# Kernel tuning notes

Measured on AMD Instinct MI355X. Metric: run time of the kernel, lower is better.

## Reference

```python
import jax, jax.numpy as jnp
import numpy as np

B, T, D, H = 2, 2048, 1024, 16
HS = D // H  # head_size = 64
EPS = 1e-5


def layer_norm(x, g, b):
    mu = jnp.mean(x, axis=-1, keepdims=True)
    var = jnp.var(x, axis=-1, keepdims=True)
    return (x - mu) * jax.lax.rsqrt(var + EPS) * g + b


def setup_inputs() -> dict:
    key = jax.random.key(0)
    ks = jax.random.split(key, 12)
    s_attn = 1.0 / np.sqrt(D)
    s_ff1 = 1.0 / np.sqrt(D)
    s_ff2 = 1.0 / np.sqrt(4 * D)
    return {
        "x": jax.random.normal(ks[0], (B, T, D), jnp.float32),
        "Wq": jax.random.normal(ks[1], (H, D, HS), jnp.float32) * s_attn,
        "Wk": jax.random.normal(ks[2], (H, D, HS), jnp.float32) * s_attn,
        "Wv": jax.random.normal(ks[3], (H, D, HS), jnp.float32) * s_attn,
        "Wo": jax.random.normal(ks[4], (H * HS, D), jnp.float32) * (1.0 / np.sqrt(H * HS)),
        "bo": jnp.zeros((D,), jnp.float32),
        "W1": jax.random.normal(ks[5], (D, 4 * D), jnp.float32) * s_ff1,
        "b1": jnp.zeros((4 * D,), jnp.float32),
        "W2": jax.random.normal(ks[6], (4 * D, D), jnp.float32) * s_ff2,
        "b2": jnp.zeros((D,), jnp.float32),
        "ln1_g": jnp.ones((D,), jnp.float32),
        "ln1_b": jnp.zeros((D,), jnp.float32),
        "ln2_g": jnp.ones((D,), jnp.float32),
        "ln2_b": jnp.zeros((D,), jnp.float32),
    }


def reference(x, Wq, Wk, Wv, Wo, bo, W1, b1, W2, b2, ln1_g, ln1_b, ln2_g, ln2_b):
    # --- self-attention on ln1(x) ---
    h = layer_norm(x, ln1_g, ln1_b)
    Q = jnp.einsum('bsd,hdk->bhsk', h, Wq)
    K = jnp.einsum('bsd,hdk->bhsk', h, Wk)
    V = jnp.einsum('bsd,hdk->bhsk', h, Wv)
    scores = jnp.einsum('bhqk,bhsk->bhqs', Q, K) * (HS ** -0.5)
    attn = jax.nn.softmax(scores, axis=-1)  # [B,H,T,T] non-causal, as in source
    out = jnp.einsum('bhqs,bhsk->bhqk', attn, V)
    out = out.transpose(0, 2, 1, 3).reshape(B, T, H * HS)  # concat heads
    sa = out @ Wo + bo
    x = x + sa
    # --- feed-forward on ln2(x) ---
    h2 = layer_norm(x, ln2_g, ln2_b)
    ff = jax.nn.relu(h2 @ W1 + b1) @ W2 + b2
    return x + ff
```

## Files before the change

kernel.cpp:

```cpp
#include <hip/hip_runtime.h>
#include <cstdint>
#include <cmath>

typedef __bf16 bf16;
typedef __bf16 bf16x8 __attribute__((ext_vector_type(8)));
typedef __bf16 bf16x4 __attribute__((ext_vector_type(4)));
typedef float  f32x4  __attribute__((ext_vector_type(4)));

#define B_   2
#define T_   2048
#define D_   1024
#define H_   16
#define HS_  64
#define NTOK (B_ * T_)

typedef __attribute__((address_space(1))) uint8_t* gp1_t;
typedef __attribute__((address_space(3))) uint8_t* lp3_t;
__device__ __forceinline__ void gl_lds16(const void* g, void* l) {
    __builtin_amdgcn_global_load_lds((gp1_t)(uintptr_t)g,
                                     (lp3_t)(uint32_t)(uintptr_t)l,
                                     16, 0, 0);
}

__device__ __forceinline__ f32x4 mfma16(bf16x8 a, bf16x8 b, f32x4 c) {
    return __builtin_amdgcn_mfma_f32_16x16x32_bf16(a, b, c, 0, 0, 0);
}

__global__ void tcast(const float* __restrict__ in, bf16* __restrict__ out,
                      int R, int C) {
    __shared__ float t[32][33];
    const int c0 = blockIdx.x * 32, r0 = blockIdx.y * 32;
    for (int i = 0; i < 4; i++) {
        int r = threadIdx.y + i * 8;
        t[r][threadIdx.x] = in[(size_t)(r0 + r) * C + c0 + threadIdx.x];
    }
    __syncthreads();
    for (int i = 0; i < 4; i++) {
        int rr = threadIdx.y + i * 8;
        out[(size_t)(c0 + rr) * R + r0 + threadIdx.x] = (bf16)t[threadIdx.x][rr];
    }
}

__global__ void qkv_pack(const float* __restrict__ Wq, const float* __restrict__ Wk,
                         const float* __restrict__ Wv, bf16* __restrict__ out) {
    const int z = blockIdx.z;
    const int qkv = z >> 4;
    const float* in = (qkv == 0 ? Wq : qkv == 1 ? Wk : Wv) + (size_t)(z & 15) * D_ * HS_;
    bf16* o = out + (size_t)z * HS_ * D_;
    __shared__ float t[32][33];
    const int c0 = blockIdx.x * 32, r0 = blockIdx.y * 32;
    for (int i = 0; i < 4; i++) {
        int r = threadIdx.y + i * 8;
        t[r][threadIdx.x] = in[(size_t)(r0 + r) * HS_ + c0 + threadIdx.x];
    }
    __syncthreads();
    for (int i = 0; i < 4; i++) {
        int rr = threadIdx.y + i * 8;
        o[(size_t)(c0 + rr) * D_ + r0 + threadIdx.x] = (bf16)t[threadIdx.x][rr];
    }
}

__global__ __launch_bounds__(256) void ln_kernel(const float* __restrict__ x,
                                                 const float* __restrict__ g,
                                                 const float* __restrict__ b,
                                                 bf16* __restrict__ out) {
    const int row = blockIdx.x;
    const int tid = threadIdx.x;
    const float4 v = ((const float4*)(x + (size_t)row * 1024))[tid];
    float s  = v.x + v.y + v.z + v.w;
    float s2 = v.x * v.x + v.y * v.y + v.z * v.z + v.w * v.w;
    for (int m = 1; m < 64; m <<= 1) {
        s  += __shfl_xor(s, m);
        s2 += __shfl_xor(s2, m);
    }
    __shared__ float rs[4], rq[4];
    const int lane = tid & 63, wv = tid >> 6;
    if (lane == 0) { rs[wv] = s; rq[wv] = s2; }
    __syncthreads();
    s  = rs[0] + rs[1] + rs[2] + rs[3];
    s2 = rq[0] + rq[1] + rq[2] + rq[3];
    const float mu   = s * (1.f / 1024.f);
    const float var  = s2 * (1.f / 1024.f) - mu * mu;
    const float rstd = rsqrtf(var + 1e-5f);
    const float4 gg = ((const float4*)g)[tid];
    const float4 bb = ((const float4*)b)[tid];
    bf16x4 o;
    o[0] = (bf16)((v.x - mu) * rstd * gg.x + bb.x);
    o[1] = (bf16)((v.y - mu) * rstd * gg.y + bb.y);
    o[2] = (bf16)((v.z - mu) * rstd * gg.z + bb.z);
    o[3] = (bf16)((v.w - mu) * rstd * gg.w + bb.w);
    *(bf16x4*)(out + (size_t)row * 1024 + tid * 4) = o;
}

__global__ __launch_bounds__(256) void combine2(const float* __restrict__ p0,
                                                const float* __restrict__ p1,
                                                const float* __restrict__ resid,
                                                const float* __restrict__ bias,
                                                float* __restrict__ out) {
    const int i4 = blockIdx.x * 256 + threadIdx.x;
    const float4 a = ((const float4*)p0)[i4];
    const float4 b = ((const float4*)p1)[i4];
    const float4 r = ((const float4*)resid)[i4];
    const float4 bb = ((const float4*)bias)[i4 & 255];
    float4 o;
    o.x = a.x + b.x + r.x + bb.x;
    o.y = a.y + b.y + r.y + bb.y;
    o.z = a.z + b.z + r.z + bb.z;
    o.w = a.w + b.w + r.w + bb.w;
    ((float4*)out)[i4] = o;
}

template <int BIAS, int RELU, int RES, int OUTBF16, int VTP = 0>
__global__ __launch_bounds__(256, 2) void gemm_bt(
    const bf16* __restrict__ A, const bf16* __restrict__ Bt,
    const float* __restrict__ bias, const float* __restrict__ resid,
    void* __restrict__ Cout, bf16* __restrict__ Vt, int M, int N, int K) {
    __shared__ __align__(16) bf16 As[2][128 * 32];
    __shared__ __align__(16) bf16 Bs[2][128 * 32];
    const int tid  = threadIdx.x;
    const int lane = tid & 63, w = tid >> 6;
    const int quad = lane >> 4, l15 = lane & 15;
    const int m0 = blockIdx.y * 128, n0 = blockIdx.x * 128;
    const int wm = (w & 1) * 64, wn = (w >> 1) * 64;

    f32x4 acc[4][4];
    for (int i = 0; i < 4; i++)
        for (int j = 0; j < 4; j++) acc[i][j] = f32x4{0.f, 0.f, 0.f, 0.f};

    const int arow = lane >> 2;
    const int acol = (lane & 3) * 8;
    const int c0 = w * 2, c1 = w * 2 + 1;

    for (int kt = 0; kt < K; kt += 64) {
        gl_lds16(A  + (size_t)(m0 + c0 * 16 + arow) * K + kt + acol,      &As[0][c0 * 512]);
        gl_lds16(A  + (size_t)(m0 + c1 * 16 + arow) * K + kt + acol,      &As[0][c1 * 512]);
        gl_lds16(A  + (size_t)(m0 + c0 * 16 + arow) * K + kt + 32 + acol, &As[1][c0 * 512]);
        gl_lds16(A  + (size_t)(m0 + c1 * 16 + arow) * K + kt + 32 + acol, &As[1][c1 * 512]);
        gl_lds16(Bt + (size_t)(n0 + c0 * 16 + arow) * K + kt + acol,      &Bs[0][c0 * 512]);
        gl_lds16(Bt + (size_t)(n0 + c1 * 16 + arow) * K + kt + acol,      &Bs[0][c1 * 512]);
        gl_lds16(Bt + (size_t)(n0 + c0 * 16 + arow) * K + kt + 32 + acol, &Bs[1][c0 * 512]);
        gl_lds16(Bt + (size_t)(n0 + c1 * 16 + arow) * K + kt + 32 + acol, &Bs[1][c1 * 512]);
        __syncthreads();
        for (int kh = 0; kh < 2; kh++) {
            bf16x8 af[4], bfr[4];
            for (int mi = 0; mi < 4; mi++)
                af[mi] = *(const bf16x8*)&As[kh][(wm + mi * 16 + l15) * 32 + quad * 8];
            for (int ni = 0; ni < 4; ni++)
                bfr[ni] = *(const bf16x8*)&Bs[kh][(wn + ni * 16 + l15) * 32 + quad * 8];
            for (int mi = 0; mi < 4; mi++)
                for (int ni = 0; ni < 4; ni++)
                    acc[mi][ni] = mfma16(af[mi], bfr[ni], acc[mi][ni]);
        }
        __syncthreads();
    }

    for (int mi = 0; mi < 4; mi++) {
        for (int ni = 0; ni < 4; ni++) {
            const int colb = n0 + wn + ni * 16 + l15;
            if (VTP && colb >= 2048) {
                const int h = (colb - 2048) >> 6, hs = (colb - 2048) & 63;
                const int row0 = m0 + wm + mi * 16 + quad * 4;
                const int b = row0 >> 11;
                bf16x4 p4;
                p4[0] = (bf16)acc[mi][ni][0];
                p4[1] = (bf16)acc[mi][ni][1];
                p4[2] = (bf16)acc[mi][ni][2];
                p4[3] = (bf16)acc[mi][ni][3];
                *(bf16x4*)&Vt[((size_t)(b * 16 + h) * 64 + hs) * T_ + (row0 & 2047)] = p4;
                continue;
            }
            const float bv = BIAS ? bias[colb] : 0.f;
            for (int r = 0; r < 4; r++) {
                const int row = m0 + wm + mi * 16 + quad * 4 + r;
                float v = acc[mi][ni][r] + bv;
                if (RELU) v = fmaxf(v, 0.f);
                if (RES)  v += resid[(size_t)row * N + colb];
                if (OUTBF16) ((bf16*)Cout)[(size_t)row * N + colb] = (bf16)v;
                else         ((float*)Cout)[(size_t)row * N + colb] = v;
            }
        }
    }
}

__global__ __launch_bounds__(256, 2) void gemm_bt_partial(
    const bf16* __restrict__ A, const bf16* __restrict__ Bt,
    float* __restrict__ Cpart, int M, int N, int K) {
    __shared__ __align__(16) bf16 As[2][128 * 32];
    __shared__ __align__(16) bf16 Bs[2][128 * 32];
    const int tid  = threadIdx.x;
    const int lane = tid & 63, w = tid >> 6;
    const int quad = lane >> 4, l15 = lane & 15;
    const int m0 = blockIdx.y * 128, n0 = blockIdx.x * 128;
    const int wm = (w & 1) * 64, wn = (w >> 1) * 64;
    const int kpb = K / gridDim.z;
    const int k0 = blockIdx.z * kpb, k1 = k0 + kpb;
    float* Cz = Cpart + (size_t)blockIdx.z * M * N;

    f32x4 acc[4][4];
    for (int i = 0; i < 4; i++)
        for (int j = 0; j < 4; j++) acc[i][j] = f32x4{0.f, 0.f, 0.f, 0.f};

    const int arow = lane >> 2;
    const int acol = (lane & 3) * 8;
    const int c0 = w * 2, c1 = w * 2 + 1;

    for (int kt = k0; kt < k1; kt += 64) {
        gl_lds16(A  + (size_t)(m0 + c0 * 16 + arow) * K + kt + acol,      &As[0][c0 * 512]);
        gl_lds16(A  + (size_t)(m0 + c1 * 16 + arow) * K + kt + acol,      &As[0][c1 * 512]);
        gl_lds16(A  + (size_t)(m0 + c0 * 16 + arow) * K + kt + 32 + acol, &As[1][c0 * 512]);
        gl_lds16(A  + (size_t)(m0 + c1 * 16 + arow) * K + kt + 32 + acol, &As[1][c1 * 512]);
        gl_lds16(Bt + (size_t)(n0 + c0 * 16 + arow) * K + kt + acol,      &Bs[0][c0 * 512]);
        gl_lds16(Bt + (size_t)(n0 + c1 * 16 + arow) * K + kt + acol,      &Bs[0][c1 * 512]);
        gl_lds16(Bt + (size_t)(n0 + c0 * 16 + arow) * K + kt + 32 + acol, &Bs[1][c0 * 512]);
        gl_lds16(Bt + (size_t)(n0 + c1 * 16 + arow) * K + kt + 32 + acol, &Bs[1][c1 * 512]);
        __syncthreads();
        for (int kh = 0; kh < 2; kh++) {
            bf16x8 af[4], bfr[4];
            for (int mi = 0; mi < 4; mi++)
                af[mi] = *(const bf16x8*)&As[kh][(wm + mi * 16 + l15) * 32 + quad * 8];
            for (int ni = 0; ni < 4; ni++)
                bfr[ni] = *(const bf16x8*)&Bs[kh][(wn + ni * 16 + l15) * 32 + quad * 8];
            for (int mi = 0; mi < 4; mi++)
                for (int ni = 0; ni < 4; ni++)
                    acc[mi][ni] = mfma16(af[mi], bfr[ni], acc[mi][ni]);
        }
        __syncthreads();
    }

    for (int mi = 0; mi < 4; mi++) {
        for (int ni = 0; ni < 4; ni++) {
            const int colb = n0 + wn + ni * 16 + l15;
            for (int r = 0; r < 4; r++) {
                const int row = m0 + wm + mi * 16 + quad * 4 + r;
                Cz[(size_t)row * N + colb] = acc[mi][ni][r];
            }
        }
    }
}

#define LSTR 68
#define NJ   (T_ / 64)
__global__ __launch_bounds__(256, 2) void flash_attn(const bf16* __restrict__ QKV,
                                                     const bf16* __restrict__ Vt,
                                                     bf16* __restrict__ attn_out) {
    const int bh = blockIdx.y, b = bh >> 4, h = bh & 15;
    const int q0 = blockIdx.x * 128;
    const int tid = threadIdx.x, lane = tid & 63, w = tid >> 6;
    const int quad = lane >> 4, l15 = lane & 15;
    __shared__ __align__(16) bf16 Ks[2][64 * LSTR];
    __shared__ __align__(16) bf16 Vs[2][64 * LSTR];
    __shared__ __align__(16) bf16 Ps[128 * LSTR];
    const bf16* Qb = QKV + (size_t)b * T_ * 3072 + h * 64;
    const bf16* Kb = QKV + (size_t)b * T_ * 3072 + 1024 + h * 64;
    const bf16* Vb = Vt  + (size_t)bh * HS_ * T_;

    const float sc = 0.125f * 1.44269504088896f;
    const int sr = tid >> 2, scc = (tid & 3) * 16;

    bf16x8 QA[2][2];
    for (int qnt = 0; qnt < 2; qnt++) {
        const size_t row = (size_t)(q0 + w * 32 + qnt * 16 + l15) * 3072;
        for (int kk = 0; kk < 2; kk++) {
            bf16x8 q = *(const bf16x8*)&Qb[row + kk * 32 + quad * 8];
            for (int i = 0; i < 8; i++) q[i] = (bf16)((float)q[i] * sc);
            QA[qnt][kk] = q;
        }
    }

    bf16x8 ones8;
    for (int i = 0; i < 8; i++) ones8[i] = (bf16)1.0f;

    f32x4 O[2][4], lacc[2];
    for (int mi = 0; mi < 2; mi++) {
        lacc[mi] = f32x4{0.f, 0.f, 0.f, 0.f};
        for (int n = 0; n < 4; n++) O[mi][n] = f32x4{0.f, 0.f, 0.f, 0.f};
    }

    *(bf16x8*)&Ks[0][sr * LSTR + scc]     = *(const bf16x8*)&Kb[(size_t)sr * 3072 + scc];
    *(bf16x8*)&Ks[0][sr * LSTR + scc + 8] = *(const bf16x8*)&Kb[(size_t)sr * 3072 + scc + 8];
    *(bf16x8*)&Vs[0][sr * LSTR + scc]     = *(const bf16x8*)&Vb[(size_t)sr * T_ + scc];
    *(bf16x8*)&Vs[0][sr * LSTR + scc + 8] = *(const bf16x8*)&Vb[(size_t)sr * T_ + scc + 8];
    __syncthreads();

    bf16x8 k0, k1, v0, v1;
    for (int j = 0; j < NJ; j++) {
        const int buf = j & 1;
        if (j + 1 < NJ) {
            const int s1 = (j + 1) * 64;
            k0 = *(const bf16x8*)&Kb[(size_t)(s1 + sr) * 3072 + scc];
            k1 = *(const bf16x8*)&Kb[(size_t)(s1 + sr) * 3072 + scc + 8];
            v0 = *(const bf16x8*)&Vb[(size_t)sr * T_ + s1 + scc];
            v1 = *(const bf16x8*)&Vb[(size_t)sr * T_ + s1 + scc + 8];
        }
        bf16x8 KB[4][2];
        for (int smt = 0; smt < 4; smt++)
            for (int kk = 0; kk < 2; kk++)
                KB[smt][kk] = *(const bf16x8*)&Ks[buf][(smt * 16 + l15) * LSTR + kk * 32 + quad * 8];
        for (int qnt = 0; qnt < 2; qnt++) {
            f32x4 ST[4];
            for (int smt = 0; smt < 4; smt++) ST[smt] = f32x4{0.f, 0.f, 0.f, 0.f};
            for (int kk = 0; kk < 2; kk++)
                for (int smt = 0; smt < 4; smt++)
                    ST[smt] = mfma16(KB[smt][kk], QA[qnt][kk], ST[smt]);
            const int prow = (w * 32 + qnt * 16 + l15) * LSTR + quad * 4;
            for (int smt = 0; smt < 4; smt++) {
                bf16x4 p4;
                p4[0] = (bf16)__builtin_amdgcn_exp2f(ST[smt][0]);
                p4[1] = (bf16)__builtin_amdgcn_exp2f(ST[smt][1]);
                p4[2] = (bf16)__builtin_amdgcn_exp2f(ST[smt][2]);
                p4[3] = (bf16)__builtin_amdgcn_exp2f(ST[smt][3]);
                *(bf16x4*)&Ps[prow + smt * 16] = p4;
            }
        }
        bf16x8 VB[4][2];
        for (int n = 0; n < 4; n++)
            for (int kk = 0; kk < 2; kk++)
                VB[n][kk] = *(const bf16x8*)&Vs[buf][(n * 16 + l15) * LSTR + kk * 32 + quad * 8];
        for (int mi = 0; mi < 2; mi++) {
            const int pr = (w * 32 + mi * 16 + l15) * LSTR + quad * 8;
            bf16x8 PA0 = *(const bf16x8*)&Ps[pr];
            bf16x8 PA1 = *(const bf16x8*)&Ps[pr + 32];
            for (int n = 0; n < 4; n++) {
                O[mi][n] = mfma16(PA0, VB[n][0], O[mi][n]);
                O[mi][n] = mfma16(PA1, VB[n][1], O[mi][n]);
            }
            lacc[mi] = mfma16(PA0, ones8, lacc[mi]);
            lacc[mi] = mfma16(PA1, ones8, lacc[mi]);
        }
        if (j + 1 < NJ) {
            *(bf16x8*)&Ks[buf ^ 1][sr * LSTR + scc]     = k0;
            *(bf16x8*)&Ks[buf ^ 1][sr * LSTR + scc + 8] = k1;
            *(bf16x8*)&Vs[buf ^ 1][sr * LSTR + scc]     = v0;
            *(bf16x8*)&Vs[buf ^ 1][sr * LSTR + scc + 8] = v1;
        }
        __syncthreads();
    }

    for (int mi = 0; mi < 2; mi++) {
        for (int r = 0; r < 4; r++) {
            const float inv = 1.f / lacc[mi][r];
            const size_t tok = (size_t)b * T_ + q0 + w * 32 + mi * 16 + quad * 4 + r;
            for (int n = 0; n < 4; n++)
                attn_out[tok * 1024 + h * 64 + n * 16 + l15] = (bf16)(O[mi][n][r] * inv);
        }
    }
}

extern "C" void kernel_launch(void* const* d_in, const int* in_sizes, int n_in,
                              void* d_out, int out_size, void* d_ws, size_t ws_size,
                              hipStream_t stream) {
    const float* x   = (const float*)d_in[0];
    const float* Wq  = (const float*)d_in[1];
    const float* Wk  = (const float*)d_in[2];
    const float* Wv  = (const float*)d_in[3];
    const float* Wo  = (const float*)d_in[4];
    const float* bo  = (const float*)d_in[5];
    const float* W1  = (const float*)d_in[6];
    const float* b1  = (const float*)d_in[7];
    const float* W2  = (const float*)d_in[8];
    const float* b2  = (const float*)d_in[9];
    const float* g1  = (const float*)d_in[10];
    const float* be1 = (const float*)d_in[11];
    const float* g2  = (const float*)d_in[12];
    const float* be2 = (const float*)d_in[13];

    char* ws = (char*)d_ws;
    const size_t MB = 1ull << 20;
    bf16*  WqkvT = (bf16*)(ws);
    bf16*  WoT   = (bf16*)(ws + 6  * MB);
    bf16*  W1T   = (bf16*)(ws + 8  * MB);
    bf16*  W2T   = (bf16*)(ws + 16 * MB);
    bf16*  hbuf  = (bf16*)(ws + 24 * MB);
    bf16*  QKV   = (bf16*)(ws + 32 * MB);
    bf16*  Vt    = (bf16*)(ws + 56 * MB);
    bf16*  attn  = (bf16*)(ws + 64 * MB);
    float* x2    = (float*)(ws + 72 * MB);
    bf16*  ff1   = (bf16*)(ws + 32 * MB);
    float* part  = (float*)(ws + 88 * MB);
    float* out   = (float*)d_out;

    dim3 tb(32, 8);
    qkv_pack<<<dim3(2, 32, 48), tb, 0, stream>>>(Wq, Wk, Wv, WqkvT);
    tcast<<<dim3(32, 32),  tb, 0, stream>>>(Wo, WoT, 1024, 1024);
    tcast<<<dim3(128, 32), tb, 0, stream>>>(W1, W1T, 1024, 4096);
    tcast<<<dim3(32, 128), tb, 0, stream>>>(W2, W2T, 4096, 1024);
    ln_kernel<<<NTOK, 256, 0, stream>>>(x, g1, be1, hbuf);
    gemm_bt<0, 0, 0, 1, 1><<<dim3(24, 32), 256, 0, stream>>>(hbuf, WqkvT, nullptr, nullptr, QKV, Vt, NTOK, 3072, 1024);
    flash_attn<<<dim3(T_ / 128, B_ * H_), 256, 0, stream>>>(QKV, Vt, attn);
    gemm_bt<1, 0, 1, 0><<<dim3(8, 32), 256, 0, stream>>>(attn, WoT, bo, x, x2, nullptr, NTOK, 1024, 1024);
    ln_kernel<<<NTOK, 256, 0, stream>>>(x2, g2, be2, hbuf);
    gemm_bt<1, 1, 0, 1><<<dim3(32, 32), 256, 0, stream>>>(hbuf, W1T, b1, nullptr, ff1, nullptr, NTOK, 4096, 1024);
    gemm_bt_partial<<<dim3(8, 32, 2), 256, 0, stream>>>(ff1, W2T, part, NTOK, 1024, 4096);
    combine2<<<NTOK, 256, 0, stream>>>(part, part + (size_t)NTOK * 1024, x2, b2, out);
}
```

Baseline: 339.9 us.

## Keep softmax probabilities in registers via permlane swaps instead of LDS round-trip

```diff
diff --git a/kernel.cpp b/kernel.cpp
--- a/kernel.cpp
+++ b/kernel.cpp
@@ -5,6 +5,7 @@
 typedef __bf16 bf16;
 typedef __bf16 bf16x8 __attribute__((ext_vector_type(8)));
 typedef __bf16 bf16x4 __attribute__((ext_vector_type(4)));
+typedef __bf16 bf16x2 __attribute__((ext_vector_type(2)));
 typedef float  f32x4  __attribute__((ext_vector_type(4)));
 
 #define B_   2
@@ -24,6 +25,17 @@
 
 __device__ __forceinline__ f32x4 mfma16(bf16x8 a, bf16x8 b, f32x4 c) {
     return __builtin_amdgcn_mfma_f32_16x16x32_bf16(a, b, c, 0, 0, 0);
+}
+
+__device__ __forceinline__ uint32_t pk2(float lo, float hi) {
+    bf16x2 t; t[0] = (bf16)lo; t[1] = (bf16)hi;
+    return __builtin_bit_cast(uint32_t, t);
+}
+__device__ __forceinline__ void pl32(uint32_t& a, uint32_t& b) {
+    asm("v_permlane32_swap_b32 %0, %1" : "+v"(a), "+v"(b));
+}
+__device__ __forceinline__ void pl16(uint32_t& a, uint32_t& b) {
+    asm("v_permlane16_swap_b32 %0, %1" : "+v"(a), "+v"(b));
 }
 
 __global__ void tcast(const float* __restrict__ in, bf16* __restrict__ out,
@@ -249,7 +261,6 @@
     const int quad = lane >> 4, l15 = lane & 15;
     __shared__ __align__(16) bf16 Ks[2][64 * LSTR];
     __shared__ __align__(16) bf16 Vs[2][64 * LSTR];
-    __shared__ __align__(16) bf16 Ps[128 * LSTR];
     const bf16* Qb = QKV + (size_t)b * T_ * 3072 + h * 64;
     const bf16* Kb = QKV + (size_t)b * T_ * 3072 + 1024 + h * 64;
     const bf16* Vb = Vt  + (size_t)bh * HS_ * T_;
@@ -293,33 +304,55 @@
             v1 = *(const bf16x8*)&Vb[(size_t)sr * T_ + s1 + scc + 8];
         }
         bf16x8 KB[4][2];
+#pragma unroll
         for (int smt = 0; smt < 4; smt++)
+#pragma unroll
             for (int kk = 0; kk < 2; kk++)
                 KB[smt][kk] = *(const bf16x8*)&Ks[buf][(smt * 16 + l15) * LSTR + kk * 32 + quad * 8];
+
+        bf16x8 PA[2][2];
+#pragma unroll
         for (int qnt = 0; qnt < 2; qnt++) {
             f32x4 ST[4];
+#pragma unroll
             for (int smt = 0; smt < 4; smt++) ST[smt] = f32x4{0.f, 0.f, 0.f, 0.f};
+            __builtin_amdgcn_s_setprio(1);
+#pragma unroll
             for (int kk = 0; kk < 2; kk++)
+#pragma unroll
                 for (int smt = 0; smt < 4; smt++)
                     ST[smt] = mfma16(KB[smt][kk], QA[qnt][kk], ST[smt]);
-            const int prow = (w * 32 + qnt * 16 + l15) * LSTR + quad * 4;
-            for (int smt = 0; smt < 4; smt++) {
-                bf16x4 p4;
-                p4[0] = (bf16)__builtin_amdgcn_exp2f(ST[smt][0]);
-                p4[1] = (bf16)__builtin_amdgcn_exp2f(ST[smt][1]);
-                p4[2] = (bf16)__builtin_amdgcn_exp2f(ST[smt][2]);
-                p4[3] = (bf16)__builtin_amdgcn_exp2f(ST[smt][3]);
-                *(bf16x4*)&Ps[prow + smt * 16] = p4;
-            }
+            __builtin_amdgcn_s_setprio(0);
+            uint32_t w00 = pk2(__builtin_amdgcn_exp2f(ST[0][0]), __builtin_amdgcn_exp2f(ST[0][1]));
+            uint32_t w01 = pk2(__builtin_amdgcn_exp2f(ST[0][2]), __builtin_amdgcn_exp2f(ST[0][3]));
+            uint32_t w10 = pk2(__builtin_amdgcn_exp2f(ST[1][0]), __builtin_amdgcn_exp2f(ST[1][1]));
+            uint32_t w11 = pk2(__builtin_amdgcn_exp2f(ST[1][2]), __builtin_amdgcn_exp2f(ST[1][3]));
+            uint32_t w20 = pk2(__builtin_amdgcn_exp2f(ST[2][0]), __builtin_amdgcn_exp2f(ST[2][1]));
+            uint32_t w21 = pk2(__builtin_amdgcn_exp2f(ST[2][2]), __builtin_amdgcn_exp2f(ST[2][3]));
+            uint32_t w30 = pk2(__builtin_amdgcn_exp2f(ST[3][0]), __builtin_amdgcn_exp2f(ST[3][1]));
+            uint32_t w31 = pk2(__builtin_amdgcn_exp2f(ST[3][2]), __builtin_amdgcn_exp2f(ST[3][3]));
+            pl32(w00, w10); pl16(w00, w10);
+            pl32(w01, w11); pl16(w01, w11);
+            pl32(w20, w30); pl16(w20, w30);
+            pl32(w21, w31); pl16(w21, w31);
+            union { uint32_t u[4]; bf16x8 v; } pa0, pa1;
+            pa0.u[0] = w00; pa0.u[1] = w01; pa0.u[2] = w10; pa0.u[3] = w11;
+            pa1.u[0] = w20; pa1.u[1] = w21; pa1.u[2] = w30; pa1.u[3] = w31;
+            PA[qnt][0] = pa0.v;
+            PA[qnt][1] = pa1.v;
         }
         bf16x8 VB[4][2];
+#pragma unroll
         for (int n = 0; n < 4; n++)
+#pragma unroll
             for (int kk = 0; kk < 2; kk++)
                 VB[n][kk] = *(const bf16x8*)&Vs[buf][(n * 16 + l15) * LSTR + kk * 32 + quad * 8];
+        __builtin_amdgcn_s_setprio(1);
+#pragma unroll
         for (int mi = 0; mi < 2; mi++) {
-            const int pr = (w * 32 + mi * 16 + l15) * LSTR + quad * 8;
-            bf16x8 PA0 = *(const bf16x8*)&Ps[pr];
-            bf16x8 PA1 = *(const bf16x8*)&Ps[pr + 32];
+            const bf16x8 PA0 = PA[mi][0];
+            const bf16x8 PA1 = PA[mi][1];
+#pragma unroll
             for (int n = 0; n < 4; n++) {
                 O[mi][n] = mfma16(PA0, VB[n][0], O[mi][n]);
                 O[mi][n] = mfma16(PA1, VB[n][1], O[mi][n]);
@@ -327,6 +360,7 @@
             lacc[mi] = mfma16(PA0, ones8, lacc[mi]);
             lacc[mi] = mfma16(PA1, ones8, lacc[mi]);
         }
+        __builtin_amdgcn_s_setprio(0);
         if (j + 1 < NJ) {
             *(bf16x8*)&Ks[buf ^ 1][sr * LSTR + scc]     = k0;
             *(bf16x8*)&Ks[buf ^ 1][sr * LSTR + scc + 8] = k1;
```

New measurement: 339.1 us. No clear change (-0.2%).
